# Kernel tuning notes

Hardware: AMD Instinct MI355X
Metric: run time of the kernel (lower is better)

The kernel has to match this reference:

```python
import jax, jax.numpy as jnp
import numpy as np

N_NODES = 65536
N_GRAPHS = 1024
NODES_PER_G = 64
N_EDGES = 1048576
IN_FEATS = 512
HIDDEN = 1024
H4 = 256
EMB = 512
EPS = 1e-5
SLOPE = 0.01


def setup_inputs() -> dict:
    key = jax.random.key(0)
    ks = jax.random.split(key, 10)
    # within-graph random edges: edge e belongs to graph e // (E/B)
    epg = N_EDGES // N_GRAPHS
    eg = np.arange(N_EDGES) // epg
    rng = np.random.default_rng(0)
    src = rng.integers(0, NODES_PER_G, N_EDGES) + eg * NODES_PER_G
    dst = rng.integers(0, NODES_PER_G, N_EDGES) + eg * NODES_PER_G
    node_gid = np.arange(N_NODES) // NODES_PER_G
    return {
        "node_feats": jax.random.normal(ks[0], (N_NODES, IN_FEATS), jnp.float32),
        "edge_weights": jax.random.uniform(ks[1], (N_EDGES,), jnp.float32),
        "W1": jax.random.normal(ks[2], (IN_FEATS, HIDDEN), jnp.float32) * 0.05,
        "W2": jax.random.normal(ks[3], (HIDDEN, H4), jnp.float32) * 0.05,
        "W_emb": jax.random.normal(ks[4], (IN_FEATS + HIDDEN + H4, EMB), jnp.float32) * 0.02,
        "gn1_alpha": jnp.ones((HIDDEN,), jnp.float32),
        "gn1_gamma": jnp.ones((HIDDEN,), jnp.float32),
        "gn1_beta": jnp.zeros((HIDDEN,), jnp.float32),
        "gn2_alpha": jnp.ones((H4,), jnp.float32),
        "gn2_gamma": jnp.ones((H4,), jnp.float32),
        "gn2_beta": jnp.zeros((H4,), jnp.float32),
        "edge_src": jnp.asarray(src, jnp.int32),
        "edge_dst": jnp.asarray(dst, jnp.int32),
        "node_gid": jnp.asarray(node_gid, jnp.int32),
    }


def _seg_sum(x, ids, num):
    return jax.ops.segment_sum(x, ids, num_segments=num)


def _graph_conv(x, W, src, dst, ew):
    # DGL GraphConv, norm='both', bias=False, with edge_weight (u_mul_e)
    ones = jnp.ones((src.shape[0],), x.dtype)
    deg_out = jnp.clip(_seg_sum(ones, src, N_NODES), 1.0)
    deg_in = jnp.clip(_seg_sum(ones, dst, N_NODES), 1.0)
    h = (x * jax.lax.rsqrt(deg_out)[:, None]) @ W
    msg = h[src] * ew[:, None]
    agg = _seg_sum(msg, dst, N_NODES)
    return agg * jax.lax.rsqrt(deg_in)[:, None]


def _graph_norm(x, gid, counts, alpha, gamma, beta):
    # GraphNorm (Cai et al.): learnable mean-scale alpha, per-graph stats
    mean = _seg_sum(x, gid, N_GRAPHS) / counts[:, None]
    sub = x - alpha * mean[gid]
    var = _seg_sum(sub * sub, gid, N_GRAPHS) / counts[:, None]
    return gamma * sub * jax.lax.rsqrt(var[gid] + EPS) + beta


def _mean_nodes(x, gid, counts):
    return _seg_sum(x, gid, N_GRAPHS) / counts[:, None]


def _leaky(x):
    return jnp.where(x >= 0, x, SLOPE * x)


def reference(node_feats, edge_weights, W1, W2, W_emb,
              gn1_alpha, gn1_gamma, gn1_beta,
              gn2_alpha, gn2_gamma, gn2_beta,
              edge_src, edge_dst, node_gid):
    counts = jnp.clip(_seg_sum(jnp.ones((N_NODES,), node_feats.dtype), node_gid, N_GRAPHS), 1.0)
    r0 = _mean_nodes(node_feats, node_gid, counts)                 # [B, in]
    h1 = _graph_conv(node_feats, W1, edge_src, edge_dst, edge_weights)
    h1 = _leaky(_graph_norm(h1, node_gid, counts, gn1_alpha, gn1_gamma, gn1_beta))
    r1 = _mean_nodes(h1, node_gid, counts)                          # [B, hidden]
    h2 = _graph_conv(h1, W2, edge_src, edge_dst, edge_weights)
    h2 = _leaky(_graph_norm(h2, node_gid, counts, gn2_alpha, gn2_gamma, gn2_beta))
    r2 = _mean_nodes(h2, node_gid, counts)                          # [B, hidden/4]
    emb = jnp.concatenate([r0, r1, r2], axis=1) @ W_emb             # [B, EMB]
    # InstanceNorm1d on [B, E] input: per-row normalization, no affine
    mu = jnp.mean(emb, axis=1, keepdims=True)
    var = jnp.mean((emb - mu) ** 2, axis=1, keepdims=True)
    emb = (emb - mu) * jax.lax.rsqrt(var + EPS)
    return _leaky(emb)
```

## Files before the change

### kernel.cpp

```cpp
#include <hip/hip_runtime.h>
#include <hip/hip_bf16.h>
#include <stdint.h>

#define N_NODES   65536
#define N_GRAPHS  1024
#define N_EDGES   1048576
#define IN_FEATS  512
#define HIDDEN    1024
#define H4        256
#define EMB_DIM   512
#define RDIM      1792
#define EPS_F     1e-5f
#define SLOPE_F   0.01f

typedef __bf16 bf16;
typedef __bf16 bf16x4 __attribute__((ext_vector_type(4)));
typedef __bf16 bf16x8 __attribute__((ext_vector_type(8)));
typedef float  floatx4 __attribute__((ext_vector_type(4)));

#define GLDS16(gp, lp) __builtin_amdgcn_global_load_lds( \
    (const __attribute__((address_space(1))) void*)(gp), \
    (__attribute__((address_space(3))) void*)(lp), 16, 0, 0)

__global__ __launch_bounds__(256) void k_graph_build(
    const int* __restrict__ src, const int* __restrict__ dst,
    const float* __restrict__ ew,
    bf16* __restrict__ adjb, float* __restrict__ scl_o)
{
    __shared__ float sAdj[4096];
    __shared__ float sDegO[64], sDegI[64];
    int g = blockIdx.x, tid = threadIdx.x;
    for (int i = tid; i < 4096; i += 256) sAdj[i] = 0.f;
    if (tid < 64) { sDegO[tid] = 0.f; sDegI[tid] = 0.f; }
    __syncthreads();
    int e0 = g * 1024;
    #pragma unroll
    for (int i = 0; i < 4; ++i) {
        int e = e0 + i * 256 + tid;
        int s = src[e] & 63, d = dst[e] & 63;
        atomicAdd(&sAdj[(d << 6) | s], ew[e]);
        atomicAdd(&sDegO[s], 1.f);
        atomicAdd(&sDegI[d], 1.f);
    }
    __syncthreads();
    if (tid < 64) scl_o[g * 64 + tid] = rsqrtf(fmaxf(sDegO[tid], 1.f));
    bf16* ag = adjb + ((size_t)g << 12);
    for (int i = tid; i < 4096; i += 256) {
        float si = rsqrtf(fmaxf(sDegI[i >> 6], 1.f));
        ag[i] = (bf16)(sAdj[i] * si);
    }
}

__global__ __launch_bounds__(256) void k_transpose(
    const float* __restrict__ W, bf16* __restrict__ WT, int K, int logN)
{
    int idx = blockIdx.x * 256 + threadIdx.x;
    if (idx >= (K << logN)) return;
    int n = idx & ((1 << logN) - 1);
    int k = idx >> logN;
    WT[(size_t)n * K + k] = (bf16)W[idx];
}

__global__ __launch_bounds__(256) void k_prep_agg1(
    const float* __restrict__ x, const float* __restrict__ so,
    const bf16* __restrict__ adjb,
    bf16* __restrict__ axs1, bf16* __restrict__ Rb)
{
    __shared__ __align__(16) bf16 sXr[64 * 260];
    __shared__ __align__(16) bf16 sOut[64 * 264];
    __shared__ float sR[4][256];
    __shared__ float sSo[64];
    int g = blockIdx.x >> 1, half = blockIdx.x & 1;
    int tid = threadIdx.x, lane = tid & 63, wave = tid >> 6, q = lane >> 4;
    if (tid < 64) sSo[tid] = so[g * 64 + tid];
    __syncthreads();

    const float* xg = x + (size_t)g * 64 * IN_FEATS + half * 256;
    const bf16* ag = adjb + ((size_t)g << 12);

    bf16x8 af[4][2];
    #pragma unroll
    for (int mt = 0; mt < 4; ++mt)
        #pragma unroll
        for (int kk = 0; kk < 2; ++kk)
            af[mt][kk] = *(const bf16x8*)&ag[(mt * 16 + (lane & 15)) * 64 + kk * 32 + q * 8];

    float r0a = 0.f, r0b = 0.f, r0c = 0.f, r0d = 0.f;
    #pragma unroll
    for (int i = 0; i < 16; ++i) {
        int row = i * 4 + wave;
        float4 v = *(const float4*)&xg[(size_t)row * IN_FEATS + lane * 4];
        r0a += v.x; r0b += v.y; r0c += v.z; r0d += v.w;
        float sc = sSo[row];
        bf16x4 p;
        p[0] = (bf16)(v.x * sc); p[1] = (bf16)(v.y * sc);
        p[2] = (bf16)(v.z * sc); p[3] = (bf16)(v.w * sc);
        *(bf16x4*)&sXr[row * 260 + lane * 4] = p;
    }
    sR[wave][lane * 4 + 0] = r0a;
    sR[wave][lane * 4 + 1] = r0b;
    sR[wave][lane * 4 + 2] = r0c;
    sR[wave][lane * 4 + 3] = r0d;
    __syncthreads();

    {
        float s = sR[0][tid] + sR[1][tid] + sR[2][tid] + sR[3][tid];
        Rb[(size_t)g * RDIM + half * 256 + tid] = (bf16)(s * (1.f / 64.f));
    }

    #pragma unroll
    for (int nt = 0; nt < 4; ++nt) {
        int cl = wave * 64 + nt * 16 + (lane & 15);
        floatx4 acc[4] = {};
        #pragma unroll
        for (int kk = 0; kk < 2; ++kk) {
            bf16x8 bfrag;
            #pragma unroll
            for (int j = 0; j < 8; ++j)
                bfrag[j] = sXr[(kk * 32 + q * 8 + j) * 260 + cl];
            #pragma unroll
            for (int mt = 0; mt < 4; ++mt)
                acc[mt] = __builtin_amdgcn_mfma_f32_16x16x32_bf16(af[mt][kk], bfrag, acc[mt], 0, 0, 0);
        }
        #pragma unroll
        for (int mt = 0; mt < 4; ++mt)
            #pragma unroll
            for (int i = 0; i < 4; ++i)
                sOut[(mt * 16 + q * 4 + i) * 264 + cl] = (bf16)acc[mt][i];
    }
    __syncthreads();
    #pragma unroll
    for (int it = 0; it < 8; ++it) {
        int idx = it * 256 + tid;
        int d = idx >> 5, c8 = idx & 31;
        *(bf16x8*)&axs1[(size_t)(g * 64 + d) * IN_FEATS + half * 256 + c8 * 8] =
            *(const bf16x8*)&sOut[d * 264 + c8 * 8];
    }
}

__global__ __launch_bounds__(512) void k_gemm12(
    const bf16* __restrict__ A, const bf16* __restrict__ BT1,
    const bf16* __restrict__ BT2, const bf16* __restrict__ adjb,
    const float* __restrict__ al1, const float* __restrict__ ga1, const float* __restrict__ be1,
    const float* __restrict__ al2, const float* __restrict__ ga2, const float* __restrict__ be2,
    const float* __restrict__ so, bf16* __restrict__ Rb)
{
    __shared__ __align__(16) bf16 sm[66560];
    __shared__ float sSo[128];
    const int tid = threadIdx.x;
    const int lane = tid & 63, wave = tid >> 6, q = lane >> 4;
    const int wm = wave >> 2, wn = wave & 3;
    const int by = blockIdx.x;
    const int row0 = by * 128;
    const int gw = by * 2 + wm;
    if (tid < 128) sSo[tid] = so[row0 + tid];

    floatx4 acc2[4][4] = {};
    bf16* sX = sm + 49152;

    #pragma unroll 1
    for (int ct = 0; ct < 8; ++ct) {
        floatx4 acc1[4][2] = {};

        auto stage_ab = [&](int k0, int buf) {
            #pragma unroll
            for (int ro = 0; ro < 2; ++ro) {
                int u = ro * 4096 + wave * 512 + lane * 8;
                int r = u >> 6, c = ((u >> 3) & 7) ^ (r & 7);
                GLDS16(A   + (size_t)(row0 + r) * IN_FEATS + k0 + c * 8,
                       sm + buf * 16384 + ro * 4096 + wave * 512);
                GLDS16(BT1 + (size_t)(ct * 128 + r) * IN_FEATS + k0 + c * 8,
                       sm + buf * 16384 + 8192 + ro * 4096 + wave * 512);
            }
        };
        auto stage_w2 = [&](int h, int buf) {
            #pragma unroll
            for (int ro = 0; ro < 4; ++ro) {
                int u = ro * 4096 + wave * 512 + lane * 8;
                int r = u >> 6, c = ((u >> 3) & 7) ^ (r & 7);
                GLDS16(BT2 + (size_t)r * HIDDEN + ct * 128 + h * 64 + c * 8,
                       sm + buf * 16384 + ro * 4096 + wave * 512);
            }
        };
        auto mfma_step = [&](int buf) {
            const bf16* sA = sm + buf * 16384;
            const bf16* sB = sA + 8192;
            #pragma unroll
            for (int kk = 0; kk < 2; ++kk) {
                bf16x8 afr[4], bfr[2];
                int cw = kk * 4 + q;
                #pragma unroll
                for (int mt = 0; mt < 4; ++mt) {
                    int r = wm * 64 + mt * 16 + (lane & 15);
                    afr[mt] = *(const bf16x8*)&sA[(r * 8 + (cw ^ (r & 7))) * 8];
                }
                #pragma unroll
                for (int nt = 0; nt < 2; ++nt) {
                    int r = wn * 32 + nt * 16 + (lane & 15);
                    bfr[nt] = *(const bf16x8*)&sB[(r * 8 + (cw ^ (r & 7))) * 8];
                }
                #pragma unroll
                for (int mt = 0; mt < 4; ++mt)
                    #pragma unroll
                    for (int nt = 0; nt < 2; ++nt)
                        acc1[mt][nt] = __builtin_amdgcn_mfma_f32_16x16x32_bf16(
                            afr[mt], bfr[nt], acc1[mt][nt], 0, 0, 0);
            }
        };

        stage_ab(0, 0);
        stage_ab(64, 1);

        #pragma unroll
        for (int t = 0; t < 8; ++t) {
            asm volatile("s_waitcnt vmcnt(4)" ::: "memory");
            __builtin_amdgcn_s_barrier();
            if (t < 6)       stage_ab((t + 2) * 64, (t + 2) % 3);
            else if (t == 6) stage_w2(0, 2);
            else             stage_w2(1, 0);
            mfma_step(t % 3);
        }

        #pragma unroll
        for (int nt = 0; nt < 2; ++nt) {
            int cl = wn * 32 + nt * 16 + (lane & 15);
            int colg = ct * 128 + cl;
            float lsum = 0.f;
            #pragma unroll
            for (int mt = 0; mt < 4; ++mt)
                #pragma unroll
                for (int i = 0; i < 4; ++i) lsum += acc1[mt][nt][i];
            lsum += __shfl_xor(lsum, 16);
            lsum += __shfl_xor(lsum, 32);
            float am = al1[colg] * (lsum * (1.f / 64.f));
            float gm = ga1[colg], bt = be1[colg];
            float sub[4][4], qv = 0.f;
            #pragma unroll
            for (int mt = 0; mt < 4; ++mt)
                #pragma unroll
                for (int i = 0; i < 4; ++i) {
                    float d = acc1[mt][nt][i] - am;
                    sub[mt][i] = d; qv += d * d;
                }
            qv += __shfl_xor(qv, 16);
            qv += __shfl_xor(qv, 32);
            float rs = rsqrtf(qv * (1.f / 64.f) + EPS_F);
            float rsum = 0.f;
            #pragma unroll
            for (int mt = 0; mt < 4; ++mt)
                #pragma unroll
                for (int i = 0; i < 4; ++i) {
                    float o = gm * sub[mt][i] * rs + bt;
                    o = (o >= 0.f) ? o : SLOPE_F * o;
                    rsum += o;
                    int r = wm * 64 + mt * 16 + q * 4 + i;
                    sX[r * 136 + cl] = (bf16)(o * sSo[r]);
                }
            rsum += __shfl_xor(rsum, 16);
            rsum += __shfl_xor(rsum, 32);
            if (lane < 16)
                Rb[(size_t)gw * RDIM + 512 + colg] = (bf16)(rsum * (1.f / 64.f));
        }
        asm volatile("s_waitcnt vmcnt(0)" ::: "memory");
        __syncthreads();

        #pragma unroll
        for (int kk2 = 0; kk2 < 4; ++kk2) {
            const bf16* sW = sm + ((kk2 < 2) ? 2 : 0) * 16384;
            int cw = (kk2 & 1) * 4 + q;
            bf16x8 afr[4], bfr[4];
            #pragma unroll
            for (int mt = 0; mt < 4; ++mt)
                afr[mt] = *(const bf16x8*)&sX[(wm * 64 + mt * 16 + (lane & 15)) * 136 + kk2 * 32 + q * 8];
            #pragma unroll
            for (int nt = 0; nt < 4; ++nt) {
                int r = wn * 64 + nt * 16 + (lane & 15);
                bfr[nt] = *(const bf16x8*)&sW[(r * 8 + (cw ^ (r & 7))) * 8];
            }
            #pragma unroll
            for (int mt = 0; mt < 4; ++mt)
                #pragma unroll
                for (int nt = 0; nt < 4; ++nt)
                    acc2[mt][nt] = __builtin_amdgcn_mfma_f32_16x16x32_bf16(
                        afr[mt], bfr[nt], acc2[mt][nt], 0, 0, 0);
        }
        __syncthreads();
    }

    bf16* sT = sm;
    #pragma unroll
    for (int nt = 0; nt < 4; ++nt) {
        int cl = wn * 64 + nt * 16 + (lane & 15);
        #pragma unroll
        for (int mt = 0; mt < 4; ++mt)
            #pragma unroll
            for (int i = 0; i < 4; ++i)
                sT[cl * 136 + wm * 64 + mt * 16 + q * 4 + i] = (bf16)acc2[mt][nt][i];
    }
    asm volatile("s_waitcnt lgkmcnt(0)" ::: "memory");

    const bf16* ag = adjb + ((size_t)gw << 12);
    floatx4 hh[4][4] = {};
    #pragma unroll
    for (int kk = 0; kk < 2; ++kk) {
        bf16x8 afr[4], bfr[4];
        #pragma unroll
        for (int mt = 0; mt < 4; ++mt)
            afr[mt] = *(const bf16x8*)&ag[(mt * 16 + (lane & 15)) * 64 + kk * 32 + q * 8];
        #pragma unroll
        for (int nt = 0; nt < 4; ++nt)
            bfr[nt] = *(const bf16x8*)&sT[(wn * 64 + nt * 16 + (lane & 15)) * 136 + wm * 64 + kk * 32 + q * 8];
        #pragma unroll
        for (int mt = 0; mt < 4; ++mt)
            #pragma unroll
            for (int nt = 0; nt < 4; ++nt)
                hh[mt][nt] = __builtin_amdgcn_mfma_f32_16x16x32_bf16(afr[mt], bfr[nt], hh[mt][nt], 0, 0, 0);
    }

    #pragma unroll
    for (int nt = 0; nt < 4; ++nt) {
        int colg = wn * 64 + nt * 16 + (lane & 15);
        float lsum = 0.f;
        #pragma unroll
        for (int mt = 0; mt < 4; ++mt)
            #pragma unroll
            for (int i = 0; i < 4; ++i) lsum += hh[mt][nt][i];
        lsum += __shfl_xor(lsum, 16);
        lsum += __shfl_xor(lsum, 32);
        float am = al2[colg] * (lsum * (1.f / 64.f));
        float gm = ga2[colg], bt = be2[colg];
        float sub[4][4], qv = 0.f;
        #pragma unroll
        for (int mt = 0; mt < 4; ++mt)
            #pragma unroll
            for (int i = 0; i < 4; ++i) {
                float d = hh[mt][nt][i] - am;
                sub[mt][i] = d; qv += d * d;
            }
        qv += __shfl_xor(qv, 16);
        qv += __shfl_xor(qv, 32);
        float rs = rsqrtf(qv * (1.f / 64.f) + EPS_F);
        float rsum = 0.f;
        #pragma unroll
        for (int mt = 0; mt < 4; ++mt)
            #pragma unroll
            for (int i = 0; i < 4; ++i) {
                float o = gm * sub[mt][i] * rs + bt;
                rsum += (o >= 0.f) ? o : SLOPE_F * o;
            }
        rsum += __shfl_xor(rsum, 16);
        rsum += __shfl_xor(rsum, 32);
        if (lane < 16)
            Rb[(size_t)gw * RDIM + 1536 + colg] = (bf16)(rsum * (1.f / 64.f));
    }
}

__device__ __forceinline__ void swizzle_block(int cb, int& bx, int& by)
{
    int b = blockIdx.y * gridDim.x + blockIdx.x;
    int xcd = b & 7, t = b >> 3;
    bx = t % cb;
    by = (t / cb) * 8 + xcd;
}

__global__ __launch_bounds__(256) void k_gemm_ro(
    const bf16* __restrict__ A, const bf16* __restrict__ BT,
    float* __restrict__ Cout)
{
    __shared__ __align__(16) bf16 sm[65536];
    const int tid = threadIdx.x;
    const int lane = tid & 63, wave = tid >> 6, q = lane >> 4;
    const int wm = wave & 1, wn = wave >> 1;
    int bx, by; swizzle_block(gridDim.x, bx, by);
    const int row0 = by * 128, col0 = bx * 128;

    floatx4 acc[4][4] = {};

    auto stage = [&](int k0, int buf) {
        #pragma unroll
        for (int i = 0; i < 4; ++i) {
            int u = (wave * 4 + i) * 64 + lane;
            int r = u >> 3, c = (u & 7) ^ (r & 7);
            GLDS16(A  + (size_t)(row0 + r) * RDIM + (k0 + c * 8),
                   sm + buf * 16384 + (wave * 4 + i) * 512);
            GLDS16(BT + (size_t)(col0 + r) * RDIM + (k0 + c * 8),
                   sm + buf * 16384 + 8192 + (wave * 4 + i) * 512);
        }
    };
    auto step = [&](int buf) {
        const bf16* sA = sm + buf * 16384;
        const bf16* sB = sA + 8192;
        #pragma unroll
        for (int kk = 0; kk < 2; ++kk) {
            bf16x8 afr[4], bfr[4];
            int cw = kk * 4 + q;
            #pragma unroll
            for (int mt = 0; mt < 4; ++mt) {
                int r = wm * 64 + mt * 16 + (lane & 15);
                afr[mt] = *(const bf16x8*)&sA[(r * 8 + (cw ^ (r & 7))) * 8];
            }
            #pragma unroll
            for (int nt = 0; nt < 4; ++nt) {
                int r = wn * 64 + nt * 16 + (lane & 15);
                bfr[nt] = *(const bf16x8*)&sB[(r * 8 + (cw ^ (r & 7))) * 8];
            }
            #pragma unroll
            for (int mt = 0; mt < 4; ++mt)
                #pragma unroll
                for (int nt = 0; nt < 4; ++nt)
                    acc[mt][nt] = __builtin_amdgcn_mfma_f32_16x16x32_bf16(
                        afr[mt], bfr[nt], acc[mt][nt], 0, 0, 0);
        }
    };

    stage(0, 0); stage(64, 1); stage(128, 2);
    #pragma unroll 1
    for (int t = 0; t < 26; ++t) {
        asm volatile("s_waitcnt vmcnt(16)" ::: "memory");
        __builtin_amdgcn_s_barrier();
        if (t < 25) stage((t + 3) * 64, (t + 3) & 3);
        step(t & 3);
    }
    asm volatile("s_waitcnt vmcnt(8)" ::: "memory");
    __builtin_amdgcn_s_barrier();
    step(2);
    asm volatile("s_waitcnt vmcnt(0)" ::: "memory");
    __builtin_amdgcn_s_barrier();
    step(3);

    #pragma unroll
    for (int mt = 0; mt < 4; ++mt)
        #pragma unroll
        for (int nt = 0; nt < 4; ++nt) {
            int col = col0 + wn * 64 + nt * 16 + (lane & 15);
            #pragma unroll
            for (int i = 0; i < 4; ++i) {
                int row = row0 + wm * 64 + mt * 16 + q * 4 + i;
                Cout[(size_t)row * EMB_DIM + col] = acc[mt][nt][i];
            }
        }
}

__global__ __launch_bounds__(256) void k_instnorm(
    const float* __restrict__ emb, float* __restrict__ out)
{
    int row = blockIdx.x, tid = threadIdx.x;
    int lane = tid & 63, wave = tid >> 6;
    __shared__ float sS[4], sQ[4];
    float v0 = emb[(size_t)row * EMB_DIM + tid];
    float v1 = emb[(size_t)row * EMB_DIM + 256 + tid];
    float s = v0 + v1, q = v0 * v0 + v1 * v1;
    #pragma unroll
    for (int off = 32; off; off >>= 1) {
        s += __shfl_down(s, off);
        q += __shfl_down(q, off);
    }
    if (lane == 0) { sS[wave] = s; sQ[wave] = q; }
    __syncthreads();
    float S = sS[0] + sS[1] + sS[2] + sS[3];
    float Q = sQ[0] + sQ[1] + sQ[2] + sQ[3];
    float mu = S * (1.f / 512.f);
    float var = Q * (1.f / 512.f) - mu * mu;
    float rs = rsqrtf(var + EPS_F);
    float o0 = (v0 - mu) * rs; o0 = (o0 >= 0.f) ? o0 : SLOPE_F * o0;
    float o1 = (v1 - mu) * rs; o1 = (o1 >= 0.f) ? o1 : SLOPE_F * o1;
    out[(size_t)row * EMB_DIM + tid]       = o0;
    out[(size_t)row * EMB_DIM + 256 + tid] = o1;
}

extern "C" void kernel_launch(void* const* d_in, const int* in_sizes, int n_in,
                              void* d_out, int out_size, void* d_ws, size_t ws_size,
                              hipStream_t stream) {
    const float* x    = (const float*)d_in[0];
    const float* ew   = (const float*)d_in[1];
    const float* W1   = (const float*)d_in[2];
    const float* W2   = (const float*)d_in[3];
    const float* Wemb = (const float*)d_in[4];
    const float* a1   = (const float*)d_in[5];
    const float* g1   = (const float*)d_in[6];
    const float* b1   = (const float*)d_in[7];
    const float* a2   = (const float*)d_in[8];
    const float* g2   = (const float*)d_in[9];
    const float* b2   = (const float*)d_in[10];
    const int* esrc   = (const int*)d_in[11];
    const int* edst   = (const int*)d_in[12];
    float* out = (float*)d_out;

    char* ws = (char*)d_ws;
    const size_t MB = 1024ull * 1024ull;
    bf16*  adjb   = (bf16*)(ws);
    float* scl_o  = (float*)(ws + 8 * MB);
    bf16*  Rb     = (bf16*)(ws + 9 * MB);
    bf16*  W1T    = (bf16*)(ws + 13 * MB);
    bf16*  W2T    = (bf16*)(ws + 14 * MB);
    bf16*  WembT  = (bf16*)(ws + 15 * MB);
    float* emb    = (float*)(ws + 17 * MB);
    bf16*  axs1   = (bf16*)(ws + 20 * MB);

    k_graph_build<<<N_GRAPHS, 256, 0, stream>>>(esrc, edst, ew, adjb, scl_o);
    k_transpose<<<2048, 256, 0, stream>>>(W1, W1T, 512, 10);
    k_transpose<<<1024, 256, 0, stream>>>(W2, W2T, 1024, 8);
    k_transpose<<<3584, 256, 0, stream>>>(Wemb, WembT, 1792, 9);

    k_prep_agg1<<<N_GRAPHS * 2, 256, 0, stream>>>(x, scl_o, adjb, axs1, Rb);

    k_gemm12<<<N_NODES / 128, 512, 0, stream>>>(
        axs1, W1T, W2T, adjb, a1, g1, b1, a2, g2, b2, scl_o, Rb);

    k_gemm_ro<<<dim3(EMB_DIM / 128, N_GRAPHS / 128), 256, 0, stream>>>(
        Rb, WembT, emb);
    k_instnorm<<<N_GRAPHS, 256, 0, stream>>>(emb, out);

    (void)in_sizes; (void)n_in; (void)out_size; (void)ws_size;
}
```

Measured before the change: 424.0 us.

## Pipeline GEMM staging across column tiles and tile the weight transposes

The fused GEMM kernel now uses a single continuous slot sequence for its A/W1 staging across all eight column tiles, so the next tile's first loads are issued before the GraphNorm epilogue and second GEMM run. W2 fragments now go straight from global memory into registers instead of through LDS, which drops the vmcnt(0) drain and one barrier per tile. The weight transpose kernels now go through a shared-memory tile, giving coalesced reads and vectorized bf16 writes. In exchange, register pressure rises from holding bfr2 (16 bf16x8 per lane), and the vmcnt wait counts are hand-tuned, so they are easy to get wrong.

Result: slower. 517.1 us (+22.0%).

```diff
diff --git a/kernel.cpp b/kernel.cpp
--- a/kernel.cpp
+++ b/kernel.cpp
@@ -51,14 +51,30 @@
     }
 }
 
-__global__ __launch_bounds__(256) void k_transpose(
-    const float* __restrict__ W, bf16* __restrict__ WT, int K, int logN)
-{
-    int idx = blockIdx.x * 256 + threadIdx.x;
-    if (idx >= (K << logN)) return;
-    int n = idx & ((1 << logN) - 1);
-    int k = idx >> logN;
-    WT[(size_t)n * K + k] = (bf16)W[idx];
+__global__ __launch_bounds__(256) void k_transpose_t(
+    const float* __restrict__ W, bf16* __restrict__ WT, int K, int N)
+{
+    __shared__ float sT[64][65];
+    const int k0 = blockIdx.x * 64, n0 = blockIdx.y * 64;
+    const int tid = threadIdx.x;
+    const int lr = tid >> 4, lc = (tid & 15) * 4;
+    #pragma unroll
+    for (int i = 0; i < 4; ++i) {
+        int row = lr + i * 16;
+        float4 v = *(const float4*)&W[(size_t)(k0 + row) * N + n0 + lc];
+        sT[row][lc + 0] = v.x; sT[row][lc + 1] = v.y;
+        sT[row][lc + 2] = v.z; sT[row][lc + 3] = v.w;
+    }
+    __syncthreads();
+    const int nn = tid >> 2, kk0 = (tid & 3) * 16;
+    #pragma unroll
+    for (int h = 0; h < 2; ++h) {
+        bf16x8 o;
+        #pragma unroll
+        for (int j = 0; j < 8; ++j)
+            o[j] = (bf16)sT[kk0 + h * 8 + j][nn];
+        *(bf16x8*)&WT[(size_t)(n0 + nn) * K + k0 + kk0 + h * 8] = o;
+    }
 }
 
 __global__ __launch_bounds__(256) void k_prep_agg1(
@@ -158,30 +174,30 @@
     floatx4 acc2[4][4] = {};
     bf16* sX = sm + 49152;
 
+    auto stage_slot = [&](int s) {
+        int k0 = (s & 7) * 64;
+        int ctp = s >> 3;
+        int buf = s % 3;
+        #pragma unroll
+        for (int ro = 0; ro < 2; ++ro) {
+            int u = ro * 4096 + wave * 512 + lane * 8;
+            int r = u >> 6, c = ((u >> 3) & 7) ^ (r & 7);
+            GLDS16(A   + (size_t)(row0 + r) * IN_FEATS + k0 + c * 8,
+                   sm + buf * 16384 + ro * 4096 + wave * 512);
+            GLDS16(BT1 + (size_t)(ctp * 128 + r) * IN_FEATS + k0 + c * 8,
+                   sm + buf * 16384 + 8192 + ro * 4096 + wave * 512);
+        }
+    };
+
+    stage_slot(0);
+    stage_slot(1);
+
     #pragma unroll 1
     for (int ct = 0; ct < 8; ++ct) {
         floatx4 acc1[4][2] = {};
-
-        auto stage_ab = [&](int k0, int buf) {
-            #pragma unroll
-            for (int ro = 0; ro < 2; ++ro) {
-                int u = ro * 4096 + wave * 512 + lane * 8;
-                int r = u >> 6, c = ((u >> 3) & 7) ^ (r & 7);
-                GLDS16(A   + (size_t)(row0 + r) * IN_FEATS + k0 + c * 8,
-                       sm + buf * 16384 + ro * 4096 + wave * 512);
-                GLDS16(BT1 + (size_t)(ct * 128 + r) * IN_FEATS + k0 + c * 8,
-                       sm + buf * 16384 + 8192 + ro * 4096 + wave * 512);
-            }
-        };
-        auto stage_w2 = [&](int h, int buf) {
-            #pragma unroll
-            for (int ro = 0; ro < 4; ++ro) {
-                int u = ro * 4096 + wave * 512 + lane * 8;
-                int r = u >> 6, c = ((u >> 3) & 7) ^ (r & 7);
-                GLDS16(BT2 + (size_t)r * HIDDEN + ct * 128 + h * 64 + c * 8,
-                       sm + buf * 16384 + ro * 4096 + wave * 512);
-            }
-        };
+        bf16x8 bfr2[4][4];
+        const int b0 = (2 * ct) % 3;
+
         auto mfma_step = [&](int buf) {
             const bf16* sA = sm + buf * 16384;
             const bf16* sB = sA + 8192;
@@ -208,17 +224,30 @@
             }
         };
 
-        stage_ab(0, 0);
-        stage_ab(64, 1);
-
         #pragma unroll
         for (int t = 0; t < 8; ++t) {
-            asm volatile("s_waitcnt vmcnt(4)" ::: "memory");
+            if (t == 0) {
+                if (ct == 0) { asm volatile("s_waitcnt vmcnt(4)" ::: "memory"); }
+                else         { asm volatile("s_waitcnt vmcnt(20)" ::: "memory"); }
+            } else if (t == 7) {
+                if (ct < 7)  { asm volatile("s_waitcnt vmcnt(20)" ::: "memory"); }
+                else         { asm volatile("s_waitcnt vmcnt(16)" ::: "memory"); }
+            } else {
+                asm volatile("s_waitcnt vmcnt(4)" ::: "memory");
+            }
             __builtin_amdgcn_s_barrier();
-            if (t < 6)       stage_ab((t + 2) * 64, (t + 2) % 3);
-            else if (t == 6) stage_w2(0, 2);
-            else             stage_w2(1, 0);
-            mfma_step(t % 3);
+            int s2 = ct * 8 + t + 2;
+            if (s2 < 64) stage_slot(s2);
+            if (t == 6) {
+                #pragma unroll
+                for (int kk2 = 0; kk2 < 4; ++kk2)
+                    #pragma unroll
+                    for (int nt = 0; nt < 4; ++nt)
+                        bfr2[kk2][nt] = *(const bf16x8*)&BT2[
+                            (size_t)(wn * 64 + nt * 16 + (lane & 15)) * HIDDEN
+                            + ct * 128 + kk2 * 32 + q * 8];
+            }
+            mfma_step((b0 + t) % 3);
         }
 
         #pragma unroll
@@ -261,31 +290,26 @@
             if (lane < 16)
                 Rb[(size_t)gw * RDIM + 512 + colg] = (bf16)(rsum * (1.f / 64.f));
         }
-        asm volatile("s_waitcnt vmcnt(0)" ::: "memory");
-        __syncthreads();
+        asm volatile("s_waitcnt lgkmcnt(0)" ::: "memory");
+        __builtin_amdgcn_s_barrier();
 
         #pragma unroll
         for (int kk2 = 0; kk2 < 4; ++kk2) {
-            const bf16* sW = sm + ((kk2 < 2) ? 2 : 0) * 16384;
-            int cw = (kk2 & 1) * 4 + q;
-            bf16x8 afr[4], bfr[4];
+            bf16x8 afr[4];
             #pragma unroll
             for (int mt = 0; mt < 4; ++mt)
                 afr[mt] = *(const bf16x8*)&sX[(wm * 64 + mt * 16 + (lane & 15)) * 136 + kk2 * 32 + q * 8];
-            #pragma unroll
-            for (int nt = 0; nt < 4; ++nt) {
-                int r = wn * 64 + nt * 16 + (lane & 15);
-                bfr[nt] = *(const bf16x8*)&sW[(r * 8 + (cw ^ (r & 7))) * 8];
-            }
             #pragma unroll
             for (int mt = 0; mt < 4; ++mt)
                 #pragma unroll
                 for (int nt = 0; nt < 4; ++nt)
                     acc2[mt][nt] = __builtin_amdgcn_mfma_f32_16x16x32_bf16(
-                        afr[mt], bfr[nt], acc2[mt][nt], 0, 0, 0);
-        }
-        __syncthreads();
-    }
+                        afr[mt], bfr2[kk2][nt], acc2[mt][nt], 0, 0, 0);
+        }
+    }
+
+    asm volatile("s_waitcnt vmcnt(0)" ::: "memory");
+    __syncthreads();
 
     bf16* sT = sm;
     #pragma unroll
@@ -498,9 +522,9 @@
     bf16*  axs1   = (bf16*)(ws + 20 * MB);
 
     k_graph_build<<<N_GRAPHS, 256, 0, stream>>>(esrc, edst, ew, adjb, scl_o);
-    k_transpose<<<2048, 256, 0, stream>>>(W1, W1T, 512, 10);
-    k_transpose<<<1024, 256, 0, stream>>>(W2, W2T, 1024, 8);
-    k_transpose<<<3584, 256, 0, stream>>>(Wemb, WembT, 1792, 9);
+    k_transpose_t<<<dim3(IN_FEATS / 64, HIDDEN / 64), 256, 0, stream>>>(W1, W1T, IN_FEATS, HIDDEN);
+    k_transpose_t<<<dim3(HIDDEN / 64, H4 / 64), 256, 0, stream>>>(W2, W2T, HIDDEN, H4);
+    k_transpose_t<<<dim3(RDIM / 64, EMB_DIM / 64), 256, 0, stream>>>(Wemb, WembT, RDIM, EMB_DIM);
 
     k_prep_agg1<<<N_GRAPHS * 2, 256, 0, stream>>>(x, scl_o, adjb, axs1, Rb);
 
```
